# Performance work log

Hardware: AMD Instinct MI355X
Metric: run time of the kernel (lower is better)

Reference implementation:

```python
import jax, jax.numpy as jnp
import numpy as np

NUM_GROUPS = 32
EPS = 1e-5


def group_norm(x, gamma, beta):
    # x: [B, C, H, W]; normalize per group of C//NUM_GROUPS channels over (c_in_group, H, W)
    B, C, H, W = x.shape
    xg = x.reshape(B, NUM_GROUPS, C // NUM_GROUPS, H, W)
    mean = jnp.mean(xg, axis=(2, 3, 4), keepdims=True)
    var = jnp.var(xg, axis=(2, 3, 4), keepdims=True)
    xn = ((xg - mean) * jax.lax.rsqrt(var + EPS)).reshape(B, C, H, W)
    return xn * gamma[None, :, None, None] + beta[None, :, None, None]


def setup_inputs() -> dict:
    key = jax.random.key(0)
    kx, kq, kp = jax.random.split(key, 3)
    B, C, H, W = 4, 256, 64, 64
    x = jax.random.normal(kx, (B, C, H, W), dtype=jnp.float32)
    gamma = jnp.ones((C,), dtype=jnp.float32)
    beta = jnp.zeros((C,), dtype=jnp.float32)
    # 1x1 convs == channel matmuls; weights [out_c, in_c]
    w_qkv = jax.random.normal(kq, (3 * C, C), dtype=jnp.float32) / np.sqrt(C)
    w_proj = jax.random.normal(kp, (C, C), dtype=jnp.float32) / np.sqrt(C)
    return {"x": x, "t": 0, "gamma": gamma, "beta": beta, "w_qkv": w_qkv, "w_proj": w_proj}


def reference(x, t, gamma, beta, w_qkv, w_proj):
    B, C, H, W = x.shape
    normed = group_norm(x, gamma, beta)  # [B,C,H,W]
    qkv = jnp.einsum('bchw,oc->bohw', normed, w_qkv)  # [B,3C,H,W]
    q, k, v = jnp.split(qkv, 3, axis=1)
    N = H * W
    q = q.reshape(B, C, N)
    k = k.reshape(B, C, N)
    v = v.reshape(B, C, N)
    # scores[b,i,j] = sum_c q[b,c,i] k[b,c,j] / sqrt(C)
    scores = jnp.einsum('bci,bcj->bij', q, k) / jnp.sqrt(jnp.asarray(C, x.dtype))
    attn = jax.nn.softmax(scores, axis=-1)  # [B,N,N]
    # out[b,c,i] = sum_j v[b,c,j] attn[b,i,j]
    out = jnp.einsum('bcj,bij->bci', v, attn).reshape(B, C, H, W)
    out = jnp.einsum('bchw,oc->bohw', out, w_proj)
    return x + out
```

## Files before the change

### kernel.cpp

```cpp
#include <hip/hip_runtime.h>

typedef __bf16 bf16x8 __attribute__((ext_vector_type(8)));
typedef float floatx4 __attribute__((ext_vector_type(4)));
typedef float floatx16 __attribute__((ext_vector_type(16)));
typedef unsigned int u32;

#define BB 4
#define CC 256
#define NN 4096

__device__ __forceinline__ unsigned short f2bf(float f) {
  union { float f; unsigned u; } v; v.f = f;
  unsigned r = v.u + 0x7fffu + ((v.u >> 16) & 1u);
  return (unsigned short)(r >> 16);
}

__device__ __forceinline__ float bf2f(unsigned short s) {
  union { unsigned u; float f; } v; v.u = ((u32)s) << 16;
  return v.f;
}

__device__ __forceinline__ void async16(const void* g, void* l) {
  __builtin_amdgcn_global_load_lds((const __attribute__((address_space(1))) u32*)g,
                                   (__attribute__((address_space(3))) u32*)l, 16, 0, 0);
}

__device__ __forceinline__ u32 fbits(float f) {
  union { float f; u32 u; } v; v.f = f; return v.u;
}

__global__ __launch_bounds__(256) void gn_stats_wconv(const float* __restrict__ x, float* __restrict__ mr,
                                                      const float* __restrict__ wqkv, const float* __restrict__ wproj,
                                                      unsigned short* __restrict__ wq_bf, unsigned short* __restrict__ wp_bf) {
  if (blockIdx.x < 1024) {
    int i = blockIdx.x * 256 + threadIdx.x;
    if (i < 196608) {
      float v = wqkv[i];
      if (i < 65536) v *= 0.090168440055560213f;
      wq_bf[i] = f2bf(v);
    } else {
      int j = i - 196608;
      wp_bf[j] = f2bf(wproj[j]);
    }
    return;
  }
  int bg = blockIdx.x - 1024;
  const float* p = x + (size_t)bg * 32768;
  int t = threadIdx.x;
  float s = 0.f, q = 0.f;
#pragma unroll
  for (int it = 0; it < 32; ++it) {
    float4 v = *(const float4*)(p + it * 1024 + t * 4);
    s += v.x + v.y + v.z + v.w;
    q += v.x * v.x + v.y * v.y + v.z * v.z + v.w * v.w;
  }
#pragma unroll
  for (int off = 1; off < 64; off <<= 1) {
    s += __shfl_xor(s, off, 64);
    q += __shfl_xor(q, off, 64);
  }
  __shared__ float red[8];
  int w = t >> 6;
  if ((t & 63) == 0) { red[w] = s; red[4 + w] = q; }
  __syncthreads();
  if (t == 0) {
    float S = red[0] + red[1] + red[2] + red[3];
    float Q = red[4] + red[5] + red[6] + red[7];
    float mean = S * (1.f / 32768.f);
    float var = Q * (1.f / 32768.f) - mean * mean;
    mr[bg] = mean;
    mr[128 + bg] = rsqrtf(var + 1e-5f);
  }
}

__global__ __launch_bounds__(256) void gn_apply(const float* __restrict__ x, const float* __restrict__ mr,
                                                const float* __restrict__ gamma, const float* __restrict__ beta,
                                                unsigned short* __restrict__ normed) {
  int bid = blockIdx.x;
  int nt = bid & 63;
  int ct = (bid >> 6) & 3;
  int b = bid >> 8;
  int c0 = ct * 64, n0 = nt * 64;
  __shared__ unsigned short T[64][80];
  int t = threadIdx.x;
#pragma unroll
  for (int it = 0; it < 4; ++it) {
    int idx = it * 256 + t;
    int cl = idx >> 4;
    int n4 = (idx & 15) * 4;
    int c = c0 + cl;
    int bg = b * 32 + (c >> 3);
    float mean = mr[bg], rstd = mr[128 + bg];
    float sc = rstd * gamma[c];
    float sh = beta[c] - mean * sc;
    float4 v = *(const float4*)(x + ((size_t)(b * CC + c)) * NN + n0 + n4);
    T[n4 + 0][cl] = f2bf(v.x * sc + sh);
    T[n4 + 1][cl] = f2bf(v.y * sc + sh);
    T[n4 + 2][cl] = f2bf(v.z * sc + sh);
    T[n4 + 3][cl] = f2bf(v.w * sc + sh);
  }
  __syncthreads();
#pragma unroll
  for (int it = 0; it < 2; ++it) {
    int idx = it * 256 + t;
    int nl = idx >> 3, ck = idx & 7;
    uint4 val;
    unsigned short* pv = (unsigned short*)&val;
#pragma unroll
    for (int j = 0; j < 8; ++j) pv[j] = T[nl][ck * 8 + j];
    *(uint4*)(normed + ((size_t)b * NN + n0 + nl) * CC + c0 + ck * 8) = val;
  }
}

__global__ __launch_bounds__(256, 2) void gemm_qkv_v(const unsigned short* __restrict__ normed,
                                                     const unsigned short* __restrict__ wq_bf,
                                                     const unsigned short* __restrict__ wv_bf,
                                                     unsigned short* __restrict__ qkbuf,
                                                     unsigned short* __restrict__ vbuf) {
  __shared__ __attribute__((aligned(16))) char smem[65536];
  int b = blockIdx.y;
  const unsigned short *Ab, *Bb;
  unsigned short* Cb;
  int ldc, m0, n0;
  if (blockIdx.x < 128) {
    int mt = blockIdx.x % 32, nt = blockIdx.x / 32;
    m0 = mt * 128; n0 = nt * 128;
    Ab = normed + (size_t)b * NN * CC + (size_t)m0 * 256;
    Bb = wq_bf + (size_t)n0 * 256;
    Cb = qkbuf + (size_t)b * NN * 512;
    ldc = 512;
  } else {
    int xx = blockIdx.x - 128;
    int mt = xx & 1, nt = xx >> 1;
    m0 = mt * 128; n0 = nt * 128;
    Ab = wv_bf + (size_t)m0 * 256;
    Bb = normed + (size_t)b * NN * CC + (size_t)n0 * 256;
    Cb = vbuf + (size_t)b * CC * NN;
    ldc = NN;
  }
  int t = threadIdx.x, w = t >> 6, l = t & 63;
  int l16 = l & 15, quad = l >> 4;
  int wr = w >> 1, wc = w & 1;

  auto stage = [&](int kb, int buf) {
    int rsub = l >> 3;
    int cj = (l & 7) ^ rsub;
    char* ab = smem + buf * 16384;
    char* bb = smem + 32768 + buf * 16384;
#pragma unroll
    for (int it = 0; it < 4; ++it) {
      int pp = w * 4 + it;
      size_t go = (size_t)(8 * pp + rsub) * 256 + kb * 64 + cj * 8;
      async16(Ab + go, ab + pp * 1024);
      async16(Bb + go, bb + pp * 1024);
    }
  };

  floatx4 acc[4][4];
#pragma unroll
  for (int m = 0; m < 4; ++m)
#pragma unroll
    for (int n = 0; n < 4; ++n)
#pragma unroll
      for (int r = 0; r < 4; ++r) acc[m][n][r] = 0.f;

  stage(0, 0);

#pragma unroll 1
  for (int kb = 0; kb < 4; ++kb) {
    int cur = kb & 1;
    __syncthreads();
    if (kb < 3) stage(kb + 1, cur ^ 1);
    const unsigned short* As = (const unsigned short*)(smem + cur * 16384);
    const unsigned short* Bs = (const unsigned short*)(smem + 32768 + cur * 16384);
#pragma unroll
    for (int kk = 0; kk < 2; ++kk) {
      bf16x8 af[4], bfr[4];
      int sw = ((kk * 4 + quad) ^ (l16 & 7)) * 8;
#pragma unroll
      for (int m = 0; m < 4; ++m)
        af[m] = *(const bf16x8*)&As[(wr * 64 + m * 16 + l16) * 64 + sw];
#pragma unroll
      for (int n = 0; n < 4; ++n)
        bfr[n] = *(const bf16x8*)&Bs[(wc * 64 + n * 16 + l16) * 64 + sw];
#pragma unroll
      for (int m = 0; m < 4; ++m)
#pragma unroll
        for (int n = 0; n < 4; ++n)
          acc[m][n] = __builtin_amdgcn_mfma_f32_16x16x32_bf16(af[m], bfr[n], acc[m][n], 0, 0, 0);
    }
  }

#pragma unroll
  for (int m = 0; m < 4; ++m)
#pragma unroll
    for (int n = 0; n < 4; ++n)
#pragma unroll
      for (int r = 0; r < 4; ++r) {
        int row = m0 + wr * 64 + m * 16 + quad * 4 + r;
        int col = n0 + wc * 64 + n * 16 + l16;
        Cb[(size_t)row * ldc + col] = f2bf(acc[m][n][r]);
      }
}

__global__ __launch_bounds__(512, 2) void attn(const unsigned short* __restrict__ qk,
                                               const unsigned short* __restrict__ vbuf,
                                               unsigned short* __restrict__ opart0,
                                               unsigned short* __restrict__ opart1,
                                               float* __restrict__ lpart) {
  __shared__ __attribute__((aligned(16))) char smem[131072];

  int xcd = blockIdx.x & 7, slot = blockIdx.x >> 3;
  int b = xcd >> 1;
  int kh = xcd & 1;
  int i0 = slot * 128;
  int k0 = kh * 32;

  int t = threadIdx.x, w = t >> 6, l = t & 63;
  int l31 = l & 31, hi = l >> 5;
  int jh = w & 1;
  int iq = w >> 1;

  const size_t bqk = (size_t)b * NN * 512;
  const size_t bv = (size_t)b * CC * NN;

  auto stage = [&](int tile, int buf) {
    const unsigned short* kg = qk + bqk + (size_t)tile * 64 * 512 + 256;
    char* kb = smem + buf * 32768;
#pragma unroll
    for (int it = 0; it < 4; ++it) {
      int pp = w * 4 + it;
      int r = 2 * pp + (l >> 5);
      int c = (l & 31) ^ (r & 31);
      async16(kg + (size_t)r * 512 + c * 8, kb + pp * 1024);
    }
    const unsigned short* vg = vbuf + bv + (size_t)tile * 64;
    char* vb = smem + 65536 + buf * 32768;
    int cj = (l & 7) ^ ((l >> 3) & 7);
#pragma unroll
    for (int it = 0; it < 4; ++it) {
      int pp = w * 4 + it;
      int rc = 8 * pp + (l >> 3);
      async16(vg + (size_t)rc * NN + cj * 8, vb + pp * 1024);
    }
  };

  stage(k0, 0);

  bf16x8 qreg[16];
  {
    const unsigned short* qp = qk + bqk + (size_t)(i0 + iq * 32 + l31) * 512 + hi * 8;
#pragma unroll
    for (int ks = 0; ks < 16; ++ks)
      qreg[ks] = *(const bf16x8*)(qp + ks * 16);
  }

  floatx16 oacc[8];
#pragma unroll
  for (int cf = 0; cf < 8; ++cf)
#pragma unroll
    for (int r = 0; r < 16; ++r) oacc[cf][r] = 0.f;
  float lacc = 0.f;

  for (int kt = 0; kt < 32; ++kt) {
    int cur = kt & 1;
    __syncthreads();
    if (kt < 31) stage(k0 + kt + 1, cur ^ 1);

    const unsigned short* Kc = (const unsigned short*)(smem + cur * 32768);
    const unsigned short* Vc = (const unsigned short*)(smem + 65536 + cur * 32768);

    floatx16 st;
#pragma unroll
    for (int r = 0; r < 16; ++r) st[r] = 0.f;
#pragma unroll
    for (int ks = 0; ks < 16; ++ks) {
      bf16x8 kf = *(const bf16x8*)&Kc[(jh * 32 + l31) * 256 + (((ks << 1) | hi) ^ l31) * 8];
      st = __builtin_amdgcn_mfma_f32_32x32x16_bf16(kf, qreg[ks], st, 0, 0, 0);
    }

    u32 pr[8];
#pragma unroll
    for (int k2 = 0; k2 < 8; ++k2) {
      float p0 = __builtin_amdgcn_exp2f(st[2 * k2]);
      float p1 = __builtin_amdgcn_exp2f(st[2 * k2 + 1]);
      lacc += p0 + p1;
      pr[k2] = __builtin_amdgcn_perm(fbits(p1), fbits(p0), 0x07060302u);
    }

    union U { u32 u[4]; bf16x8 v; } a0, a1;
    {
      u32 sA = hi ? pr[0] : pr[2], sB = hi ? pr[1] : pr[3];
      u32 rA = (u32)__shfl_xor((int)sA, 32, 64);
      u32 rB = (u32)__shfl_xor((int)sB, 32, 64);
      a0.u[0] = hi ? rA : pr[0]; a0.u[1] = hi ? rB : pr[1];
      a0.u[2] = hi ? pr[2] : rA; a0.u[3] = hi ? pr[3] : rB;
      sA = hi ? pr[4] : pr[6]; sB = hi ? pr[5] : pr[7];
      rA = (u32)__shfl_xor((int)sA, 32, 64);
      rB = (u32)__shfl_xor((int)sB, 32, 64);
      a1.u[0] = hi ? rA : pr[4]; a1.u[1] = hi ? rB : pr[5];
      a1.u[2] = hi ? pr[6] : rA; a1.u[3] = hi ? pr[7] : rB;
    }

#pragma unroll
    for (int cf = 0; cf < 8; ++cf) {
      const unsigned short* vrow = Vc + (cf * 32 + l31) * 64;
      bf16x8 v0 = *(const bf16x8*)(vrow + (((jh * 4) | hi) ^ (l31 & 7)) * 8);
      oacc[cf] = __builtin_amdgcn_mfma_f32_32x32x16_bf16(a0.v, v0, oacc[cf], 0, 0, 0);
      bf16x8 v1 = *(const bf16x8*)(vrow + (((jh * 4 + 2) | hi) ^ (l31 & 7)) * 8);
      oacc[cf] = __builtin_amdgcn_mfma_f32_32x32x16_bf16(a1.v, v1, oacc[cf], 0, 0, 0);
    }
  }

  float l2 = lacc + __shfl_xor(lacc, 32, 64);

  float* Of = (float*)smem + iq * 8192;
  __syncthreads();
  if (jh == 1) {
#pragma unroll
    for (int cf = 0; cf < 8; ++cf)
#pragma unroll
      for (int r = 0; r < 16; ++r) {
        int il = (r & 3) + 8 * (r >> 2) + 4 * hi;
        Of[il * 256 + cf * 32 + l31] = oacc[cf][r];
      }
  }
  __syncthreads();
  unsigned short* ops = kh ? opart1 : opart0;
  size_t rowbase = (size_t)b * NN + i0 + iq * 32;
  if (jh == 0) {
#pragma unroll
    for (int cf = 0; cf < 8; ++cf)
#pragma unroll
      for (int r = 0; r < 16; ++r) {
        int il = (r & 3) + 8 * (r >> 2) + 4 * hi;
        float v = oacc[cf][r] + Of[il * 256 + cf * 32 + l31];
        ops[(rowbase + il) * CC + cf * 32 + l31] = f2bf(v);
      }
  }
  __syncthreads();
  float* Lred = (float*)smem;
  if (hi == 0) Lred[w * 32 + l31] = l2;
  __syncthreads();
  if (jh == 0 && hi == 0) {
    size_t pbl = (size_t)(b * 2 + kh) * NN + i0;
    lpart[pbl + iq * 32 + l31] = Lred[(iq * 2) * 32 + l31] + Lred[(iq * 2 + 1) * 32 + l31];
  }
}

__global__ __launch_bounds__(256, 2) void gemm_proj(const unsigned short* __restrict__ wp,
                                                    const unsigned short* __restrict__ op0,
                                                    const unsigned short* __restrict__ op1,
                                                    const float* __restrict__ lp,
                                                    float* __restrict__ out, const float* __restrict__ x) {
  __shared__ __attribute__((aligned(16))) char smem[51456];
  int mt = blockIdx.x & 1;
  int nt = blockIdx.x >> 1;
  int b = blockIdx.y;
  int m0 = mt * 128, n0 = nt * 64;
  int t = threadIdx.x, w = t >> 6, l = t & 63;
  int l16 = l & 15, quad = l >> 4;
  int wr = w >> 1, wc = w & 1;
  const unsigned short* Ab = wp + (size_t)m0 * 256;
  float* Linv = (float*)(smem + 51200);

  auto stageA = [&](int kb, int buf) {
    int rsub = l >> 3;
    int cj = (l & 7) ^ rsub;
    char* ab = smem + buf * 16384;
#pragma unroll
    for (int it = 0; it < 4; ++it) {
      int pp = w * 4 + it;
      size_t go = (size_t)(8 * pp + rsub) * 256 + kb * 64 + cj * 8;
      async16(Ab + go, ab + pp * 1024);
    }
  };

  int brow = t >> 2;
  int bck = (t & 3) * 16;
  size_t bgo_base = ((size_t)b * NN + n0 + brow) * 256 + bck;
  uint4 b0a, b0b, b1a, b1b;
  auto loadB = [&](int kb) {
    size_t go = bgo_base + kb * 64;
    b0a = *(const uint4*)(op0 + go);
    b0b = *(const uint4*)(op0 + go + 8);
    b1a = *(const uint4*)(op1 + go);
    b1b = *(const uint4*)(op1 + go + 8);
  };

  if (t < 64) Linv[t] = 1.f / (lp[b * 8192 + n0 + t] + lp[b * 8192 + 4096 + n0 + t]);
  stageA(0, 0);
  loadB(0);
  __syncthreads();

  floatx4 acc[4][2];
#pragma unroll
  for (int m = 0; m < 4; ++m)
#pragma unroll
    for (int n = 0; n < 2; ++n)
#pragma unroll
      for (int r = 0; r < 4; ++r) acc[m][n][r] = 0.f;

#pragma unroll 1
  for (int kb = 0; kb < 4; ++kb) {
    int cur = kb & 1;
    {
      float li = Linv[brow];
      unsigned short* Bs = (unsigned short*)(smem + 32768 + cur * 9216);
      const unsigned short* pa = (const unsigned short*)&b0a;
      const unsigned short* pc = (const unsigned short*)&b1a;
      union { unsigned short us[8]; uint4 q; } o1_, o2_;
#pragma unroll
      for (int j = 0; j < 8; ++j) o1_.us[j] = f2bf((bf2f(pa[j]) + bf2f(pc[j])) * li);
      pa = (const unsigned short*)&b0b;
      pc = (const unsigned short*)&b1b;
#pragma unroll
      for (int j = 0; j < 8; ++j) o2_.us[j] = f2bf((bf2f(pa[j]) + bf2f(pc[j])) * li);
      *(uint4*)&Bs[brow * 72 + bck] = o1_.q;
      *(uint4*)&Bs[brow * 72 + bck + 8] = o2_.q;
    }
    if (kb < 3) loadB(kb + 1);
    __syncthreads();
    if (kb < 3) stageA(kb + 1, cur ^ 1);
    const unsigned short* As = (const unsigned short*)(smem + cur * 16384);
    const unsigned short* Bs = (const unsigned short*)(smem + 32768 + cur * 9216);
#pragma unroll
    for (int kk = 0; kk < 2; ++kk) {
      bf16x8 af[4], bfr[2];
      int sw = ((kk * 4 + quad) ^ (l16 & 7)) * 8;
#pragma unroll
      for (int m = 0; m < 4; ++m)
        af[m] = *(const bf16x8*)&As[(wr * 64 + m * 16 + l16) * 64 + sw];
#pragma unroll
      for (int n = 0; n < 2; ++n)
        bfr[n] = *(const bf16x8*)&Bs[(wc * 32 + n * 16 + l16) * 72 + kk * 32 + quad * 8];
#pragma unroll
      for (int m = 0; m < 4; ++m)
#pragma unroll
        for (int n = 0; n < 2; ++n)
          acc[m][n] = __builtin_amdgcn_mfma_f32_16x16x32_bf16(af[m], bfr[n], acc[m][n], 0, 0, 0);
    }
  }

  size_t cb = (size_t)b * CC * NN;
#pragma unroll
  for (int m = 0; m < 4; ++m)
#pragma unroll
    for (int n = 0; n < 2; ++n)
#pragma unroll
      for (int r = 0; r < 4; ++r) {
        int row = m0 + wr * 64 + m * 16 + quad * 4 + r;
        int col = n0 + wc * 32 + n * 16 + l16;
        size_t idx = cb + (size_t)row * NN + col;
        out[idx] = acc[m][n][r] + x[idx];
      }
}

extern "C" void kernel_launch(void* const* d_in, const int* in_sizes, int n_in,
                              void* d_out, int out_size, void* d_ws, size_t ws_size,
                              hipStream_t stream) {
  const float* x     = (const float*)d_in[0];
  const float* gamma = (const float*)d_in[2];
  const float* beta  = (const float*)d_in[3];
  const float* wqkv  = (const float*)d_in[4];
  const float* wproj = (const float*)d_in[5];
  float* out = (float*)d_out;

  char* p = (char*)d_ws;
  float* mr               = (float*)(p + 0);
  unsigned short* wq_bf   = (unsigned short*)(p + 1024);
  unsigned short* wp_bf   = (unsigned short*)(p + 394240);
  unsigned short* normed  = (unsigned short*)(p + 525312);
  unsigned short* qkbuf   = (unsigned short*)(p + 8913920);
  unsigned short* vbuf    = (unsigned short*)(p + 25691136);
  unsigned short* opart1  = (unsigned short*)(p + 34079744);
  unsigned short* opart0  = normed;
  float* lpart            = (float*)(p + 1024);
  unsigned short* wv_bf   = wq_bf + 512 * 256;

  gn_stats_wconv<<<1152, 256, 0, stream>>>(x, mr, wqkv, wproj, wq_bf, wp_bf);
  gn_apply<<<1024, 256, 0, stream>>>(x, mr, gamma, beta, normed);
  gemm_qkv_v<<<dim3(192, 4), 256, 0, stream>>>(normed, wq_bf, wv_bf, qkbuf, vbuf);
  attn<<<256, 512, 0, stream>>>(qkbuf, vbuf, opart0, opart1, lpart);
  gemm_proj<<<dim3(128, 4), 256, 0, stream>>>(wp_bf, opart0, opart1, lpart, out, x);
}
```

Baseline: 187.9 us.

## Fuse group-norm statistics and apply into one kernel using LDS staging

Merges the stats kernel and the normalize/transpose kernel into one kernel where each block handles one (batch, group). The block caches the group's inputs as bf16 in LDS while reducing, then normalizes from LDS and writes channel-last output. This avoids re-reading x from global memory and removes one launch. In exchange it uses only 128 blocks with large LDS footprints, and it adds a double rounding (x to bf16 before the affine) plus strided 16-byte output writes.

```diff
diff --git a/kernel.cpp b/kernel.cpp
--- a/kernel.cpp
+++ b/kernel.cpp
@@ -4,6 +4,7 @@
 typedef float floatx4 __attribute__((ext_vector_type(4)));
 typedef float floatx16 __attribute__((ext_vector_type(16)));
 typedef unsigned int u32;
+typedef unsigned long long u64;
 
 #define BB 4
 #define CC 256
@@ -29,86 +30,84 @@
   union { float f; u32 u; } v; v.f = f; return v.u;
 }
 
-__global__ __launch_bounds__(256) void gn_stats_wconv(const float* __restrict__ x, float* __restrict__ mr,
-                                                      const float* __restrict__ wqkv, const float* __restrict__ wproj,
-                                                      unsigned short* __restrict__ wq_bf, unsigned short* __restrict__ wp_bf) {
-  if (blockIdx.x < 1024) {
-    int i = blockIdx.x * 256 + threadIdx.x;
-    if (i < 196608) {
-      float v = wqkv[i];
-      if (i < 65536) v *= 0.090168440055560213f;
-      wq_bf[i] = f2bf(v);
-    } else {
-      int j = i - 196608;
-      wp_bf[j] = f2bf(wproj[j]);
+__global__ __launch_bounds__(256) void gn_fused(const float* __restrict__ x,
+                                                const float* __restrict__ gamma, const float* __restrict__ beta,
+                                                unsigned short* __restrict__ normed,
+                                                const float* __restrict__ wqkv, const float* __restrict__ wproj,
+                                                unsigned short* __restrict__ wq_bf, unsigned short* __restrict__ wp_bf) {
+  int t = threadIdx.x;
+  if (blockIdx.x >= 128) {
+    int base = (blockIdx.x - 128) * 1024;
+#pragma unroll
+    for (int j = 0; j < 4; ++j) {
+      int i = base + j * 256 + t;
+      if (i < 196608) {
+        float v = wqkv[i];
+        if (i < 65536) v *= 0.090168440055560213f;
+        wq_bf[i] = f2bf(v);
+      } else {
+        wp_bf[i - 196608] = f2bf(wproj[i - 196608]);
+      }
     }
     return;
   }
-  int bg = blockIdx.x - 1024;
+
+  __shared__ __attribute__((aligned(16))) char smem[65928];
+  unsigned short* xs = (unsigned short*)smem;
+  float* par = (float*)(smem + 65664);
+
+  int bg = blockIdx.x;
+  int b = bg >> 5, g = bg & 31;
   const float* p = x + (size_t)bg * 32768;
-  int t = threadIdx.x;
   float s = 0.f, q = 0.f;
 #pragma unroll
   for (int it = 0; it < 32; ++it) {
-    float4 v = *(const float4*)(p + it * 1024 + t * 4);
+    int idx = it * 1024 + t * 4;
+    float4 v = *(const float4*)(p + idx);
     s += v.x + v.y + v.z + v.w;
     q += v.x * v.x + v.y * v.y + v.z * v.z + v.w * v.w;
+    u64 pk = (u64)f2bf(v.x) | ((u64)f2bf(v.y) << 16) | ((u64)f2bf(v.z) << 32) | ((u64)f2bf(v.w) << 48);
+    int row = idx >> 12, col = idx & 4095;
+    *(u64*)&xs[row * 4104 + col] = pk;
   }
 #pragma unroll
   for (int off = 1; off < 64; off <<= 1) {
     s += __shfl_xor(s, off, 64);
     q += __shfl_xor(q, off, 64);
   }
-  __shared__ float red[8];
   int w = t >> 6;
-  if ((t & 63) == 0) { red[w] = s; red[4 + w] = q; }
+  if ((t & 63) == 0) { par[32 + w] = s; par[40 + w] = q; }
   __syncthreads();
   if (t == 0) {
-    float S = red[0] + red[1] + red[2] + red[3];
-    float Q = red[4] + red[5] + red[6] + red[7];
+    float S = par[32] + par[33] + par[34] + par[35];
+    float Q = par[40] + par[41] + par[42] + par[43];
     float mean = S * (1.f / 32768.f);
     float var = Q * (1.f / 32768.f) - mean * mean;
-    mr[bg] = mean;
-    mr[128 + bg] = rsqrtf(var + 1e-5f);
-  }
-}
-
-__global__ __launch_bounds__(256) void gn_apply(const float* __restrict__ x, const float* __restrict__ mr,
-                                                const float* __restrict__ gamma, const float* __restrict__ beta,
-                                                unsigned short* __restrict__ normed) {
-  int bid = blockIdx.x;
-  int nt = bid & 63;
-  int ct = (bid >> 6) & 3;
-  int b = bid >> 8;
-  int c0 = ct * 64, n0 = nt * 64;
-  __shared__ unsigned short T[64][80];
-  int t = threadIdx.x;
-#pragma unroll
-  for (int it = 0; it < 4; ++it) {
-    int idx = it * 256 + t;
-    int cl = idx >> 4;
-    int n4 = (idx & 15) * 4;
-    int c = c0 + cl;
-    int bg = b * 32 + (c >> 3);
-    float mean = mr[bg], rstd = mr[128 + bg];
-    float sc = rstd * gamma[c];
-    float sh = beta[c] - mean * sc;
-    float4 v = *(const float4*)(x + ((size_t)(b * CC + c)) * NN + n0 + n4);
-    T[n4 + 0][cl] = f2bf(v.x * sc + sh);
-    T[n4 + 1][cl] = f2bf(v.y * sc + sh);
-    T[n4 + 2][cl] = f2bf(v.z * sc + sh);
-    T[n4 + 3][cl] = f2bf(v.w * sc + sh);
-  }
-  __syncthreads();
-#pragma unroll
-  for (int it = 0; it < 2; ++it) {
-    int idx = it * 256 + t;
-    int nl = idx >> 3, ck = idx & 7;
-    uint4 val;
-    unsigned short* pv = (unsigned short*)&val;
-#pragma unroll
-    for (int j = 0; j < 8; ++j) pv[j] = T[nl][ck * 8 + j];
-    *(uint4*)(normed + ((size_t)b * NN + n0 + nl) * CC + c0 + ck * 8) = val;
+    par[16] = mean;
+    par[17] = rsqrtf(var + 1e-5f);
+  }
+  __syncthreads();
+  if (t < 8) {
+    float mean = par[16], rstd = par[17];
+    float sc = rstd * gamma[g * 8 + t];
+    par[t] = sc;
+    par[8 + t] = beta[g * 8 + t] - mean * sc;
+  }
+  __syncthreads();
+  float scv[8], shv[8];
+#pragma unroll
+  for (int c = 0; c < 8; ++c) { scv[c] = par[c]; shv[c] = par[8 + c]; }
+  unsigned short* ob = normed + ((size_t)b * NN) * CC + g * 8;
+#pragma unroll
+  for (int k = 0; k < 16; ++k) {
+    int n = k * 256 + t;
+    union { unsigned short us[8]; uint4 qv; } o;
+#pragma unroll
+    for (int c = 0; c < 8; ++c) {
+      float xv = bf2f(xs[c * 4104 + n]);
+      o.us[c] = f2bf(xv * scv[c] + shv[c]);
+    }
+    *(uint4*)(ob + (size_t)n * CC) = o.qv;
   }
 }
 
@@ -467,7 +466,6 @@
   float* out = (float*)d_out;
 
   char* p = (char*)d_ws;
-  float* mr               = (float*)(p + 0);
   unsigned short* wq_bf   = (unsigned short*)(p + 1024);
   unsigned short* wp_bf   = (unsigned short*)(p + 394240);
   unsigned short* normed  = (unsigned short*)(p + 525312);
@@ -478,8 +476,7 @@
   float* lpart            = (float*)(p + 1024);
   unsigned short* wv_bf   = wq_bf + 512 * 256;
 
-  gn_stats_wconv<<<1152, 256, 0, stream>>>(x, mr, wqkv, wproj, wq_bf, wp_bf);
-  gn_apply<<<1024, 256, 0, stream>>>(x, mr, gamma, beta, normed);
+  gn_fused<<<384, 256, 0, stream>>>(x, gamma, beta, normed, wqkv, wproj, wq_bf, wp_bf);
   gemm_qkv_v<<<dim3(192, 4), 256, 0, stream>>>(normed, wq_bf, wv_bf, qkbuf, vbuf);
   attn<<<256, 512, 0, stream>>>(qkbuf, vbuf, opart0, opart1, lpart);
   gemm_proj<<<dim3(128, 4), 256, 0, stream>>>(wp_bf, opart0, opart1, lpart, out, x);
```

Result: no change. 186.0 us (-1.0%).
